# Kernel optimization log

Hardware: AMD Instinct MI355X
Metric: run time of the kernel (lower is better)

## Reference

```python
import jax, jax.numpy as jnp
import numpy as np

B, H, W, C_IN, F = 4, 64, 64, 128, 256


def setup_inputs() -> dict:
    key = jax.random.key(0)
    ks = jax.random.split(key, 6)
    return {
        "inputs": jax.random.normal(ks[0], (B, H, W, C_IN), dtype=jnp.float32),
        "W_proj": jax.random.normal(ks[1], (C_IN, F), dtype=jnp.float32) * 0.02,
        "b_proj": jnp.zeros((F,), dtype=jnp.float32),
        "W_q": jax.random.normal(ks[2], (F, F), dtype=jnp.float32) * 0.02,
        "b_q": jnp.zeros((F,), dtype=jnp.float32),
        "W_k": jax.random.normal(ks[3], (F, F), dtype=jnp.float32) * 0.02,
        "b_k": jnp.zeros((F,), dtype=jnp.float32),
        "W_v": jax.random.normal(ks[4], (F, F), dtype=jnp.float32) * 0.02,
        "b_v": jnp.zeros((F,), dtype=jnp.float32),
        "gamma": jax.random.uniform(ks[5], (1,), dtype=jnp.float32),
    }


def reference(inputs, W_proj, b_proj, W_q, b_q, W_k, b_k, W_v, b_v, gamma):
    # 1x1 conv projection (C_in -> filters) since input channels != filters
    x = jnp.einsum("bhwc,cf->bhwf", inputs, W_proj) + b_proj  # [B,H,W,F]
    q = jnp.einsum("bhwf,fg->bhwg", x, W_q) + b_q
    k = jnp.einsum("bhwf,fg->bhwg", x, W_k) + b_k
    v = jnp.einsum("bhwf,fg->bhwg", x, W_v) + b_v
    b, h, w, f = x.shape
    n = h * w
    qr = q.reshape(b, n, f)
    kr = k.reshape(b, n, f)
    vr = v.reshape(b, n, f)
    attn = jax.nn.softmax(jnp.einsum("bnf,bmf->bnm", qr, kr), axis=-1)  # [B,N,N]
    context = jnp.einsum("bnm,bmf->bnf", attn, vr).reshape(b, h, w, f)
    return gamma * context + x
```

## Files before the change

kernel.cpp:

```cpp
#include <hip/hip_runtime.h>
#include <hip/hip_bf16.h>
#include <stdint.h>

typedef __attribute__((ext_vector_type(8))) short short8;
typedef __attribute__((ext_vector_type(4))) float floatx4;

#define DEVI __device__ __forceinline__
#define MFMA16(a, b, c) __builtin_amdgcn_mfma_f32_16x16x32_bf16((a), (b), (c), 0, 0, 0)
#define MFMA8(a, b, c)  __builtin_amdgcn_mfma_f32_16x16x32_fp8_fp8((a), (b), (c), 0, 0, 0)

typedef __attribute__((address_space(3))) unsigned int lds_u32;
typedef __attribute__((address_space(1))) const unsigned int glb_u32;
#define GLOAD_LDS16(g, l) __builtin_amdgcn_global_load_lds((glb_u32*)(g), (lds_u32*)(l), 16, 0, 0)

DEVI unsigned short f2bf(float x) {
    union { float f; unsigned int u; } v; v.f = x;
    unsigned int r = v.u + 0x7FFFu + ((v.u >> 16) & 1u);
    return (unsigned short)(r >> 16);
}
DEVI float bf2f(unsigned short h) {
    union { unsigned int u; float f; } v; v.u = ((unsigned int)h) << 16;
    return v.f;
}
DEVI unsigned char f2fp8(float x) {
    int c = __builtin_amdgcn_cvt_pk_fp8_f32(x, x, 0, false);
    return (unsigned char)(c & 0xFF);
}


__global__ void cast_f32_bf16(const float* __restrict__ in, unsigned short* __restrict__ out, int n4) {
    int i = blockIdx.x * blockDim.x + threadIdx.x;
    if (i < n4) {
        float4 v = ((const float4*)in)[i];
        ushort4 o;
        o.x = f2bf(v.x); o.y = f2bf(v.y); o.z = f2bf(v.z); o.w = f2bf(v.w);
        ((ushort4*)out)[i] = o;
    }
}

__global__ void transpose_cast(const float* __restrict__ W, unsigned short* __restrict__ Wt, int K, int N) {
    int idx = blockIdx.x * blockDim.x + threadIdx.x;
    if (idx < K * N) {
        int k = idx / N, n = idx % N;
        Wt[n * K + k] = f2bf(W[idx]);
    }
}

__global__ __launch_bounds__(256) void pack_k8(unsigned char* __restrict__ kb) {
    __shared__ unsigned char T[64][272];
    const int b = blockIdx.y, k0 = blockIdx.x * 64;
    unsigned char* base = kb + (size_t)b * 1048576 + (size_t)k0 * 256;
    const int tid = threadIdx.x;
    #pragma unroll
    for (int it = 0; it < 4; ++it) {
        int idx = tid + it * 256;
        int row = idx >> 4, col = (idx & 15) * 16;
        *(int4*)&T[row][col] = *(const int4*)&base[(size_t)row * 256 + col];
    }
    __syncthreads();
    const int w = tid >> 6, lane = tid & 63, l15 = lane & 15, quad = lane >> 4;
    #pragma unroll
    for (int s = 0; s < 8; ++s) {
        long o = *(const long*)&T[w * 16 + l15][s * 32 + quad * 8];
        *(long*)&base[(size_t)(w * 8 + s) * 512 + lane * 8] = o;
    }
}

__global__ __launch_bounds__(256) void pack_v8(unsigned char* __restrict__ vb) {
    __shared__ unsigned char T[64][272];
    const int b = blockIdx.y, k0 = blockIdx.x * 64;
    unsigned char* base = vb + (size_t)b * 1048576 + (size_t)k0 * 256;
    const int tid = threadIdx.x;
    #pragma unroll
    for (int it = 0; it < 4; ++it) {
        int idx = tid + it * 256;
        int row = idx >> 4, col = (idx & 15) * 16;
        *(int4*)&T[row][col] = *(const int4*)&base[(size_t)row * 256 + col];
    }
    __syncthreads();
    const int w = tid >> 6, lane = tid & 63, l15 = lane & 15, quad = lane >> 4;
    const int ncl = w >> 1;
    #pragma unroll
    for (int ff = 0; ff < 8; ++ff) {
        int f16 = (w & 1) * 8 + ff;
        union { unsigned char bts[8]; long l; } o;
        #pragma unroll
        for (int j = 0; j < 8; ++j)
            o.bts[j] = T[ncl * 32 + quad * 8 + j][f16 * 16 + l15];
        *(long*)&base[(size_t)(ncl * 16 + f16) * 512 + lane * 8] = o.l;
    }
}


template<int K>
__global__ __launch_bounds__(256) void gemm_bias(
    const unsigned short* __restrict__ A,
    const unsigned short* __restrict__ Wt,
    const float* __restrict__ bias,
    unsigned short* __restrict__ Cb,
    int M, int N)
{
    __shared__ unsigned short As[64][136];
    __shared__ unsigned short Bs[64][136];
    const int tid  = threadIdx.x;
    const int w    = tid >> 6;
    const int lane = tid & 63;
    const int quad = lane >> 4;
    const int l15  = lane & 15;
    const int m0 = blockIdx.x * 64;
    const int n0 = blockIdx.y * 64;

    floatx4 acc[4];
    #pragma unroll
    for (int t = 0; t < 4; ++t) acc[t] = (floatx4)0.0f;

    for (int kc = 0; kc < K; kc += 128) {
        __syncthreads();
        #pragma unroll
        for (int idx = tid; idx < 1024; idx += 256) {
            int r = idx >> 4, g = idx & 15;
            *(short8*)&As[r][g * 8] = *(const short8*)&A[(size_t)(m0 + r) * K + kc + g * 8];
            *(short8*)&Bs[r][g * 8] = *(const short8*)&Wt[(size_t)(n0 + r) * K + kc + g * 8];
        }
        __syncthreads();
        #pragma unroll
        for (int s = 0; s < 4; ++s) {
            short8 a = *(const short8*)&As[w * 16 + l15][s * 32 + quad * 8];
            #pragma unroll
            for (int t = 0; t < 4; ++t) {
                short8 bfr = *(const short8*)&Bs[t * 16 + l15][s * 32 + quad * 8];
                acc[t] = MFMA16(a, bfr, acc[t]);
            }
        }
    }

    #pragma unroll
    for (int t = 0; t < 4; ++t) {
        int n = n0 + t * 16 + l15;
        float bs = bias[n];
        #pragma unroll
        for (int r = 0; r < 4; ++r) {
            int m = m0 + w * 16 + quad * 4 + r;
            Cb[(size_t)m * N + n] = f2bf(acc[t][r] + bs);
        }
    }
}

__global__ __launch_bounds__(256) void gemm_qkv(
    const unsigned short* __restrict__ A,
    const unsigned short* __restrict__ Wt0, const unsigned short* __restrict__ Wt1, const unsigned short* __restrict__ Wt2,
    const float* __restrict__ b0, const float* __restrict__ b1, const float* __restrict__ b2,
    unsigned char* __restrict__ C0, unsigned char* __restrict__ C1, unsigned char* __restrict__ C2,
    int M, int N)
{
    const unsigned short* Wt = (blockIdx.z == 0) ? Wt0 : (blockIdx.z == 1) ? Wt1 : Wt2;
    const float* bias        = (blockIdx.z == 0) ? b0  : (blockIdx.z == 1) ? b1  : b2;
    unsigned char* Cb        = (blockIdx.z == 0) ? C0  : (blockIdx.z == 1) ? C1  : C2;

    __shared__ unsigned short As[64][136];
    __shared__ unsigned short Bs[64][136];
    const int tid  = threadIdx.x;
    const int w    = tid >> 6;
    const int lane = tid & 63;
    const int quad = lane >> 4;
    const int l15  = lane & 15;
    const int m0 = blockIdx.x * 64;
    const int n0 = blockIdx.y * 64;

    floatx4 acc[4];
    #pragma unroll
    for (int t = 0; t < 4; ++t) acc[t] = (floatx4)0.0f;

    for (int kc = 0; kc < 256; kc += 128) {
        __syncthreads();
        #pragma unroll
        for (int idx = tid; idx < 1024; idx += 256) {
            int r = idx >> 4, g = idx & 15;
            *(short8*)&As[r][g * 8] = *(const short8*)&A[(size_t)(m0 + r) * 256 + kc + g * 8];
            *(short8*)&Bs[r][g * 8] = *(const short8*)&Wt[(size_t)(n0 + r) * 256 + kc + g * 8];
        }
        __syncthreads();
        #pragma unroll
        for (int s = 0; s < 4; ++s) {
            short8 a = *(const short8*)&As[w * 16 + l15][s * 32 + quad * 8];
            #pragma unroll
            for (int t = 0; t < 4; ++t) {
                short8 bfr = *(const short8*)&Bs[t * 16 + l15][s * 32 + quad * 8];
                acc[t] = MFMA16(a, bfr, acc[t]);
            }
        }
    }

    #pragma unroll
    for (int t = 0; t < 4; ++t) {
        int n = n0 + t * 16 + l15;
        float bs = bias[n];
        #pragma unroll
        for (int r = 0; r < 4; ++r) {
            int m = m0 + w * 16 + quad * 4 + r;
            Cb[(size_t)m * N + n] = f2fp8(acc[t][r] + bs);
        }
    }
}


__global__ __launch_bounds__(256, 2) void flash_attn(
    const unsigned char* __restrict__ qg,
    const unsigned char* __restrict__ kp,
    const unsigned char* __restrict__ vp,
    const unsigned short* __restrict__ xb,
    const float* __restrict__ gamma,
    float* __restrict__ out)
{
    __shared__ __align__(16) unsigned char KV[2][32768];
    __shared__ unsigned char Ps[4][16][48];
    float* MbF = (float*)&KV[0][0];
    float* Ml  = MbF + 32 * 260;

    const int tid  = threadIdx.x;
    const int w    = tid >> 6;
    const int lane = tid & 63;
    const int quad = lane >> 4;
    const int l15  = lane & 15;
    const int rw   = w & 1;
    const int kh   = w >> 1;
    const int blk  = blockIdx.x;
    const int b    = (blk & 7) >> 1;
    const int rt   = (blk >> 3) * 2 + (blk & 1);
    const int row0 = rt * 32 + rw * 16;

    const size_t baseQ = ((size_t)b * 4096 + row0 + l15) * 256;
    long qf[8];
    #pragma unroll
    for (int s = 0; s < 8; ++s)
        qf[s] = *(const long*)&qg[baseQ + s * 32 + quad * 8];

    const long ones8 = 0x3838383838383838L;

    floatx4 ctx[16];
    #pragma unroll
    for (int i = 0; i < 16; ++i) ctx[i] = (floatx4)0.0f;
    floatx4 lacc = (floatx4)0.0f;

    const unsigned char* kb_all = kp + (size_t)b * 1048576;
    const unsigned char* vb_all = vp + (size_t)b * 1048576;

#define FA_STAGE(T, BUF)                                                             \
    {                                                                                \
        _Pragma("unroll")                                                            \
        for (int p = 0; p < 8; ++p) {                                                \
            const int c    = p * 4 + w;                                              \
            const int ckh  = c >> 4;                                                 \
            const int csel = (c >> 3) & 1;                                           \
            const int coff = (c & 7) * 1024;                                         \
            const unsigned char* src = (csel ? vb_all : kb_all)                      \
                + (size_t)ckh * 524288 + (size_t)(T) * 8192 + coff + lane * 16;      \
            GLOAD_LDS16(src, &KV[BUF][ckh * 16384 + csel * 8192 + coff]);            \
        }                                                                            \
    }

    FA_STAGE(0, 0)

    for (int t = 0; t < 64; ++t) {
        const int buf = t & 1;
        __syncthreads();
        if (t < 63) FA_STAGE(t + 1, buf ^ 1)

        const unsigned char* kc = &KV[buf][kh * 16384];
        const unsigned char* vc = &KV[buf][kh * 16384 + 8192];

        floatx4 sac0 = (floatx4)0.0f, sac1 = (floatx4)0.0f;
        #pragma unroll
        for (int s = 0; s < 8; ++s) {
            long kf0 = *(const long*)&kc[(size_t)s * 512 + lane * 8];
            long kf1 = *(const long*)&kc[(size_t)(8 + s) * 512 + lane * 8];
            sac0 = MFMA8(qf[s], kf0, sac0);
            sac1 = MFMA8(qf[s], kf1, sac1);
        }

        #pragma unroll
        for (int r = 0; r < 4; ++r) {
            Ps[w][quad * 4 + r][l15]      = f2fp8(__expf(sac0[r]));
            Ps[w][quad * 4 + r][16 + l15] = f2fp8(__expf(sac1[r]));
        }

        long ap = *(const long*)&Ps[w][l15][quad * 8];
        lacc = MFMA8(ap, ones8, lacc);
        #pragma unroll
        for (int fi = 0; fi < 16; ++fi) {
            long vfrag = *(const long*)&vc[(size_t)fi * 512 + lane * 8];
            ctx[fi] = MFMA8(ap, vfrag, ctx[fi]);
        }
    }
#undef FA_STAGE

    __syncthreads();
    if (kh == 1) {
        #pragma unroll
        for (int fi = 0; fi < 16; ++fi) {
            #pragma unroll
            for (int r = 0; r < 4; ++r)
                MbF[(rw * 16 + quad * 4 + r) * 260 + fi * 16 + l15] = ctx[fi][r];
        }
        if (l15 == 0) {
            #pragma unroll
            for (int r = 0; r < 4; ++r) Ml[rw * 16 + quad * 4 + r] = lacc[r];
        }
    }
    __syncthreads();
    if (kh == 0) {
        #pragma unroll
        for (int fi = 0; fi < 16; ++fi) {
            #pragma unroll
            for (int r = 0; r < 4; ++r)
                MbF[(rw * 16 + quad * 4 + r) * 260 + fi * 16 + l15] += ctx[fi][r];
        }
        if (l15 == 0) {
            #pragma unroll
            for (int r = 0; r < 4; ++r) Ml[rw * 16 + quad * 4 + r] += lacc[r];
        }
    }
    __syncthreads();

    const float g = gamma[0];
    const int row = tid >> 3;
    const int c0  = (tid & 7) * 32;
    const float rl = 1.0f / Ml[row];
    const size_t o = ((size_t)b * 4096 + rt * 32 + row) * 256 + c0;
    #pragma unroll
    for (int j = 0; j < 4; ++j) {
        short8 xv = *(const short8*)&xb[o + j * 8];
        float res[8];
        #pragma unroll
        for (int i = 0; i < 8; ++i)
            res[i] = g * MbF[row * 260 + c0 + j * 8 + i] * rl + bf2f((unsigned short)xv[i]);
        *(float4*)&out[o + j * 8]     = *(float4*)&res[0];
        *(float4*)&out[o + j * 8 + 4] = *(float4*)&res[4];
    }
}


extern "C" void kernel_launch(void* const* d_in, const int* in_sizes, int n_in,
                              void* d_out, int out_size, void* d_ws, size_t ws_size,
                              hipStream_t stream)
{
    const float* inp   = (const float*)d_in[0];
    const float* Wp    = (const float*)d_in[1];
    const float* bp    = (const float*)d_in[2];
    const float* Wq    = (const float*)d_in[3];
    const float* bq    = (const float*)d_in[4];
    const float* Wk    = (const float*)d_in[5];
    const float* bk    = (const float*)d_in[6];
    const float* Wv    = (const float*)d_in[7];
    const float* bv    = (const float*)d_in[8];
    const float* gamma = (const float*)d_in[9];
    float* out = (float*)d_out;

    char* ws = (char*)d_ws;
    unsigned char*  q8    = (unsigned char*)(ws + 0);
    unsigned char*  k8    = (unsigned char*)(ws + 4194304);
    unsigned char*  v8    = (unsigned char*)(ws + 8388608);
    unsigned short* x_b   = (unsigned short*)(ws + 12582912);
    unsigned short* in_b  = (unsigned short*)(ws + 20971520);
    unsigned short* Wt_p  = (unsigned short*)(ws + 25165824);
    unsigned short* Wt_q  = (unsigned short*)(ws + 25231360);
    unsigned short* Wt_k  = (unsigned short*)(ws + 25362432);
    unsigned short* Wt_v  = (unsigned short*)(ws + 25493504);

    cast_f32_bf16<<<2048, 256, 0, stream>>>(inp, in_b, 2097152 / 4);
    transpose_cast<<<128, 256, 0, stream>>>(Wp, Wt_p, 128, 256);
    transpose_cast<<<256, 256, 0, stream>>>(Wq, Wt_q, 256, 256);
    transpose_cast<<<256, 256, 0, stream>>>(Wk, Wt_k, 256, 256);
    transpose_cast<<<256, 256, 0, stream>>>(Wv, Wt_v, 256, 256);

    gemm_bias<128><<<dim3(256, 4), 256, 0, stream>>>(in_b, Wt_p, bp, x_b, 16384, 256);
    gemm_qkv<<<dim3(256, 4, 3), 256, 0, stream>>>(x_b, Wt_q, Wt_k, Wt_v, bq, bk, bv,
                                                  q8, k8, v8, 16384, 256);
    pack_k8<<<dim3(64, 4), 256, 0, stream>>>(k8);
    pack_v8<<<dim3(64, 4), 256, 0, stream>>>(v8);

    flash_attn<<<512, 256, 0, stream>>>(q8, k8, v8, x_b, gamma, out);
}
```

Baseline: 205.2 us.

## Switch flash attention to 32x32x16 fp8 MFMA with 512-thread blocks and 4-way key split

```diff
diff --git a/kernel.cpp b/kernel.cpp
--- a/kernel.cpp
+++ b/kernel.cpp
@@ -4,10 +4,11 @@
 
 typedef __attribute__((ext_vector_type(8))) short short8;
 typedef __attribute__((ext_vector_type(4))) float floatx4;
+typedef __attribute__((ext_vector_type(16))) float floatx16;
 
 #define DEVI __device__ __forceinline__
 #define MFMA16(a, b, c) __builtin_amdgcn_mfma_f32_16x16x32_bf16((a), (b), (c), 0, 0, 0)
-#define MFMA8(a, b, c)  __builtin_amdgcn_mfma_f32_16x16x32_fp8_fp8((a), (b), (c), 0, 0, 0)
+#define MFMA32(a, b, c) __builtin_amdgcn_mfma_f32_32x32x16_fp8_fp8((a), (b), (c), 0, 0, 0)
 
 typedef __attribute__((address_space(3))) unsigned int lds_u32;
 typedef __attribute__((address_space(1))) const unsigned int glb_u32;
@@ -48,8 +49,8 @@
 
 __global__ __launch_bounds__(256) void pack_k8(unsigned char* __restrict__ kb) {
     __shared__ unsigned char T[64][272];
-    const int b = blockIdx.y, k0 = blockIdx.x * 64;
-    unsigned char* base = kb + (size_t)b * 1048576 + (size_t)k0 * 256;
+    const int b = blockIdx.y, blk = blockIdx.x;
+    unsigned char* base = kb + (size_t)b * 1048576 + (size_t)blk * 16384;
     const int tid = threadIdx.x;
     #pragma unroll
     for (int it = 0; it < 4; ++it) {
@@ -58,18 +59,20 @@
         *(int4*)&T[row][col] = *(const int4*)&base[(size_t)row * 256 + col];
     }
     __syncthreads();
-    const int w = tid >> 6, lane = tid & 63, l15 = lane & 15, quad = lane >> 4;
-    #pragma unroll
-    for (int s = 0; s < 8; ++s) {
-        long o = *(const long*)&T[w * 16 + l15][s * 32 + quad * 8];
-        *(long*)&base[(size_t)(w * 8 + s) * 512 + lane * 8] = o;
+    const int w = tid >> 6, lane = tid & 63, l31 = lane & 31, hi = lane >> 5;
+    const int tile = w >> 1, sh = (w & 1) * 8;
+    #pragma unroll
+    for (int i = 0; i < 8; ++i) {
+        int s = sh + i;
+        long o = *(const long*)&T[tile * 32 + l31][s * 16 + hi * 8];
+        *(long*)&base[(size_t)tile * 8192 + (size_t)s * 512 + lane * 8] = o;
     }
 }
 
 __global__ __launch_bounds__(256) void pack_v8(unsigned char* __restrict__ vb) {
     __shared__ unsigned char T[64][272];
-    const int b = blockIdx.y, k0 = blockIdx.x * 64;
-    unsigned char* base = vb + (size_t)b * 1048576 + (size_t)k0 * 256;
+    const int b = blockIdx.y, blk = blockIdx.x;
+    unsigned char* base = vb + (size_t)b * 1048576 + (size_t)blk * 16384;
     const int tid = threadIdx.x;
     #pragma unroll
     for (int it = 0; it < 4; ++it) {
@@ -78,16 +81,17 @@
         *(int4*)&T[row][col] = *(const int4*)&base[(size_t)row * 256 + col];
     }
     __syncthreads();
-    const int w = tid >> 6, lane = tid & 63, l15 = lane & 15, quad = lane >> 4;
-    const int ncl = w >> 1;
-    #pragma unroll
-    for (int ff = 0; ff < 8; ++ff) {
-        int f16 = (w & 1) * 8 + ff;
+    const int w = tid >> 6, lane = tid & 63, l31 = lane & 31, hi = lane >> 5;
+    const int tile = w >> 1, hw = w & 1;
+    #pragma unroll
+    for (int i = 0; i < 8; ++i) {
+        int c = hw * 8 + i;
+        int fb = c >> 1, s2 = c & 1;
         union { unsigned char bts[8]; long l; } o;
         #pragma unroll
         for (int j = 0; j < 8; ++j)
-            o.bts[j] = T[ncl * 32 + quad * 8 + j][f16 * 16 + l15];
-        *(long*)&base[(size_t)(ncl * 16 + f16) * 512 + lane * 8] = o.l;
+            o.bts[j] = T[tile * 32 + s2 * 16 + hi * 8 + j][fb * 32 + l31];
+        *(long*)&base[(size_t)tile * 8192 + (size_t)c * 512 + lane * 8] = o.l;
     }
 }
 
@@ -204,7 +208,7 @@
 }
 
 
-__global__ __launch_bounds__(256, 2) void flash_attn(
+__global__ __launch_bounds__(512, 2) void flash_attn(
     const unsigned char* __restrict__ qg,
     const unsigned char* __restrict__ kp,
     const unsigned char* __restrict__ vp,
@@ -212,128 +216,139 @@
     const float* __restrict__ gamma,
     float* __restrict__ out)
 {
-    __shared__ __align__(16) unsigned char KV[2][32768];
-    __shared__ unsigned char Ps[4][16][48];
+    __shared__ __align__(16) unsigned char KV[2][65536];
     float* MbF = (float*)&KV[0][0];
-    float* Ml  = MbF + 32 * 260;
+    float* Ml  = MbF + 64 * 264;
 
     const int tid  = threadIdx.x;
     const int w    = tid >> 6;
     const int lane = tid & 63;
-    const int quad = lane >> 4;
-    const int l15  = lane & 15;
-    const int rw   = w & 1;
-    const int kh   = w >> 1;
+    const int l31  = lane & 31;
+    const int hi   = lane >> 5;
+    const int kq   = w & 3;
+    const int rw   = w >> 2;
     const int blk  = blockIdx.x;
     const int b    = (blk & 7) >> 1;
     const int rt   = (blk >> 3) * 2 + (blk & 1);
-    const int row0 = rt * 32 + rw * 16;
-
-    const size_t baseQ = ((size_t)b * 4096 + row0 + l15) * 256;
-    long qf[8];
-    #pragma unroll
-    for (int s = 0; s < 8; ++s)
-        qf[s] = *(const long*)&qg[baseQ + s * 32 + quad * 8];
+    const int row0 = rt * 64 + rw * 32;
+
+    const size_t baseQ = ((size_t)b * 4096 + row0 + l31) * 256 + hi * 8;
+    long qf[16];
+    #pragma unroll
+    for (int s = 0; s < 16; ++s)
+        qf[s] = *(const long*)&qg[baseQ + s * 16];
 
     const long ones8 = 0x3838383838383838L;
 
-    floatx4 ctx[16];
-    #pragma unroll
-    for (int i = 0; i < 16; ++i) ctx[i] = (floatx4)0.0f;
-    floatx4 lacc = (floatx4)0.0f;
-
-    const unsigned char* kb_all = kp + (size_t)b * 1048576;
-    const unsigned char* vb_all = vp + (size_t)b * 1048576;
+    floatx16 ctx[8];
+    #pragma unroll
+    for (int i = 0; i < 8; ++i) ctx[i] = (floatx16)0.0f;
+    floatx16 lacc = (floatx16)0.0f;
+
+    const unsigned char* kb_b = kp + (size_t)b * 1048576;
+    const unsigned char* vb_b = vp + (size_t)b * 1048576;
 
 #define FA_STAGE(T, BUF)                                                             \
     {                                                                                \
         _Pragma("unroll")                                                            \
         for (int p = 0; p < 8; ++p) {                                                \
-            const int c    = p * 4 + w;                                              \
-            const int ckh  = c >> 4;                                                 \
+            const int c    = p * 8 + w;                                              \
+            const int ckq  = c >> 4;                                                 \
             const int csel = (c >> 3) & 1;                                           \
             const int coff = (c & 7) * 1024;                                         \
-            const unsigned char* src = (csel ? vb_all : kb_all)                      \
-                + (size_t)ckh * 524288 + (size_t)(T) * 8192 + coff + lane * 16;      \
-            GLOAD_LDS16(src, &KV[BUF][ckh * 16384 + csel * 8192 + coff]);            \
+            const unsigned char* src = (csel ? vb_b : kb_b)                          \
+                + (size_t)ckq * 262144 + (size_t)(T) * 8192 + coff + lane * 16;      \
+            GLOAD_LDS16(src, &KV[BUF][ckq * 16384 + csel * 8192 + coff]);            \
         }                                                                            \
     }
 
     FA_STAGE(0, 0)
 
-    for (int t = 0; t < 64; ++t) {
+    for (int t = 0; t < 32; ++t) {
         const int buf = t & 1;
         __syncthreads();
-        if (t < 63) FA_STAGE(t + 1, buf ^ 1)
-
-        const unsigned char* kc = &KV[buf][kh * 16384];
-        const unsigned char* vc = &KV[buf][kh * 16384 + 8192];
-
-        floatx4 sac0 = (floatx4)0.0f, sac1 = (floatx4)0.0f;
-        #pragma unroll
-        for (int s = 0; s < 8; ++s) {
-            long kf0 = *(const long*)&kc[(size_t)s * 512 + lane * 8];
-            long kf1 = *(const long*)&kc[(size_t)(8 + s) * 512 + lane * 8];
-            sac0 = MFMA8(qf[s], kf0, sac0);
-            sac1 = MFMA8(qf[s], kf1, sac1);
-        }
-
-        #pragma unroll
-        for (int r = 0; r < 4; ++r) {
-            Ps[w][quad * 4 + r][l15]      = f2fp8(__expf(sac0[r]));
-            Ps[w][quad * 4 + r][16 + l15] = f2fp8(__expf(sac1[r]));
-        }
-
-        long ap = *(const long*)&Ps[w][l15][quad * 8];
-        lacc = MFMA8(ap, ones8, lacc);
-        #pragma unroll
-        for (int fi = 0; fi < 16; ++fi) {
-            long vfrag = *(const long*)&vc[(size_t)fi * 512 + lane * 8];
-            ctx[fi] = MFMA8(ap, vfrag, ctx[fi]);
+        if (t < 31) FA_STAGE(t + 1, buf ^ 1)
+
+        const unsigned char* kc = &KV[buf][kq * 16384];
+        const unsigned char* vc = &KV[buf][kq * 16384 + 8192];
+
+        floatx16 sa = (floatx16)0.0f, sb = (floatx16)0.0f;
+        #pragma unroll
+        for (int s = 0; s < 16; s += 2) {
+            long k0 = *(const long*)&kc[(size_t)s * 512 + lane * 8];
+            long k1 = *(const long*)&kc[(size_t)(s + 1) * 512 + lane * 8];
+            sa = MFMA32(k0, qf[s], sa);
+            sb = MFMA32(k1, qf[s + 1], sb);
+        }
+
+        float e[16];
+        #pragma unroll
+        for (int r = 0; r < 16; ++r) e[r] = __expf(sa[r] + sb[r]);
+        int X0 = __builtin_amdgcn_cvt_pk_fp8_f32(e[0],  e[1],  0,  false);
+        X0     = __builtin_amdgcn_cvt_pk_fp8_f32(e[2],  e[3],  X0, true);
+        int Y0 = __builtin_amdgcn_cvt_pk_fp8_f32(e[4],  e[5],  0,  false);
+        Y0     = __builtin_amdgcn_cvt_pk_fp8_f32(e[6],  e[7],  Y0, true);
+        int X1 = __builtin_amdgcn_cvt_pk_fp8_f32(e[8],  e[9],  0,  false);
+        X1     = __builtin_amdgcn_cvt_pk_fp8_f32(e[10], e[11], X1, true);
+        int Y1 = __builtin_amdgcn_cvt_pk_fp8_f32(e[12], e[13], 0,  false);
+        Y1     = __builtin_amdgcn_cvt_pk_fp8_f32(e[14], e[15], Y1, true);
+        asm volatile("v_permlane32_swap_b32 %0, %1" : "+v"(X0), "+v"(Y0));
+        asm volatile("v_permlane32_swap_b32 %0, %1" : "+v"(X1), "+v"(Y1));
+        union { int i2[2]; long l; } u0, u1;
+        u0.i2[0] = X0; u0.i2[1] = Y0;
+        u1.i2[0] = X1; u1.i2[1] = Y1;
+        const long ap0 = u0.l;
+        const long ap1 = u1.l;
+
+        lacc = MFMA32(ap0, ones8, lacc);
+        lacc = MFMA32(ap1, ones8, lacc);
+        #pragma unroll
+        for (int fb = 0; fb < 8; ++fb) {
+            long v0 = *(const long*)&vc[(size_t)(fb * 2)     * 512 + lane * 8];
+            long v1 = *(const long*)&vc[(size_t)(fb * 2 + 1) * 512 + lane * 8];
+            ctx[fb] = MFMA32(ap0, v0, ctx[fb]);
+            ctx[fb] = MFMA32(ap1, v1, ctx[fb]);
         }
     }
 #undef FA_STAGE
 
     __syncthreads();
-    if (kh == 1) {
-        #pragma unroll
-        for (int fi = 0; fi < 16; ++fi) {
+    for (int pass = 3; pass >= 0; --pass) {
+        if (kq == pass) {
             #pragma unroll
-            for (int r = 0; r < 4; ++r)
-                MbF[(rw * 16 + quad * 4 + r) * 260 + fi * 16 + l15] = ctx[fi][r];
-        }
-        if (l15 == 0) {
-            #pragma unroll
-            for (int r = 0; r < 4; ++r) Ml[rw * 16 + quad * 4 + r] = lacc[r];
-        }
-    }
-    __syncthreads();
-    if (kh == 0) {
-        #pragma unroll
-        for (int fi = 0; fi < 16; ++fi) {
-            #pragma unroll
-            for (int r = 0; r < 4; ++r)
-                MbF[(rw * 16 + quad * 4 + r) * 260 + fi * 16 + l15] += ctx[fi][r];
-        }
-        if (l15 == 0) {
-            #pragma unroll
-            for (int r = 0; r < 4; ++r) Ml[rw * 16 + quad * 4 + r] += lacc[r];
-        }
-    }
-    __syncthreads();
+            for (int fb = 0; fb < 8; ++fb) {
+                #pragma unroll
+                for (int r = 0; r < 16; ++r) {
+                    int row = rw * 32 + (r & 3) + 8 * (r >> 2) + 4 * hi;
+                    int idx = row * 264 + fb * 32 + l31;
+                    float prev = (pass == 3) ? 0.0f : MbF[idx];
+                    MbF[idx] = prev + ctx[fb][r];
+                }
+            }
+            if (l31 == 0) {
+                #pragma unroll
+                for (int r = 0; r < 16; ++r) {
+                    int row = rw * 32 + (r & 3) + 8 * (r >> 2) + 4 * hi;
+                    float prev = (pass == 3) ? 0.0f : Ml[row];
+                    Ml[row] = prev + lacc[r];
+                }
+            }
+        }
+        __syncthreads();
+    }
 
     const float g = gamma[0];
     const int row = tid >> 3;
     const int c0  = (tid & 7) * 32;
     const float rl = 1.0f / Ml[row];
-    const size_t o = ((size_t)b * 4096 + rt * 32 + row) * 256 + c0;
+    const size_t o = ((size_t)b * 4096 + rt * 64 + row) * 256 + c0;
     #pragma unroll
     for (int j = 0; j < 4; ++j) {
         short8 xv = *(const short8*)&xb[o + j * 8];
         float res[8];
         #pragma unroll
         for (int i = 0; i < 8; ++i)
-            res[i] = g * MbF[row * 260 + c0 + j * 8 + i] * rl + bf2f((unsigned short)xv[i]);
+            res[i] = g * MbF[row * 264 + c0 + j * 8 + i] * rl + bf2f((unsigned short)xv[i]);
         *(float4*)&out[o + j * 8]     = *(float4*)&res[0];
         *(float4*)&out[o + j * 8 + 4] = *(float4*)&res[4];
     }
@@ -379,5 +394,5 @@
     pack_k8<<<dim3(64, 4), 256, 0, stream>>>(k8);
     pack_v8<<<dim3(64, 4), 256, 0, stream>>>(v8);
 
-    flash_attn<<<512, 256, 0, stream>>>(q8, k8, v8, x_b, gamma, out);
-}
+    flash_attn<<<256, 512, 0, stream>>>(q8, k8, v8, x_b, gamma, out);
+}
```

After: 206.7 us. Within noise of the previous version (+0.7%).
